# Optimization experiments

Hardware: AMD Instinct MI355X
Metric: run time of the kernel (lower is better)

The kernel has to match this reference:

```python
import jax, jax.numpy as jnp
import numpy as np


def setup_inputs() -> dict:
    key = jax.random.key(0)
    k1, k2, k3, k4 = jax.random.split(key, 4)
    N, M, D, C = 8192, 8192, 512, 128
    ref_feats = jax.random.normal(k1, (N, D), dtype=jnp.float32)
    src_feats = jax.random.normal(k2, (M, D), dtype=jnp.float32)
    # pairwise_distance(..., normalized=True) assumes unit-norm features
    ref_feats = ref_feats / jnp.linalg.norm(ref_feats, axis=-1, keepdims=True)
    src_feats = src_feats / jnp.linalg.norm(src_feats, axis=-1, keepdims=True)
    cas_score0 = jax.random.uniform(k3, (C, N), dtype=jnp.float32)
    cas_score1 = jax.random.uniform(k4, (C, M), dtype=jnp.float32)
    return {
        "ref_feats": ref_feats,
        "src_feats": src_feats,
        "cas_score0": cas_score0,
        "cas_score1": cas_score1,
        "num_correspondences": 256,
    }


def reference(ref_feats, src_feats, cas_score0, cas_score1, num_correspondences):
    # masks are None -> all superpoints kept, ref_indices/src_indices = arange
    N = ref_feats.shape[0]
    M = src_feats.shape[0]
    # pairwise_distance(normalized=True): d = 2 - 2 * <ref, src>
    inner = jnp.einsum('nd,md->nm', ref_feats, src_feats)
    matching_scores = jnp.exp(-(2.0 - 2.0 * inner))  # [N, M]
    # dual normalization (row-wise and col-wise)
    ref_ms = matching_scores / jnp.sum(matching_scores, axis=1, keepdims=True)
    src_ms = matching_scores / jnp.sum(matching_scores, axis=0, keepdims=True)
    matching_scores = ref_ms * src_ms
    # overlap matrix: [N, M]
    overlap = jnp.einsum('cn,cm->nm', cas_score0, cas_score1)
    matching_scores = matching_scores * overlap
    k = min(num_correspondences, N * M)
    corr_scores, corr_indices = jax.lax.top_k(matching_scores.reshape(-1), k)
    ref_corr_indices = corr_indices // M
    src_corr_indices = corr_indices % M
    return ref_corr_indices, src_corr_indices, corr_scores
```

## Files before the change

### kernel.cpp

```cpp
#include <hip/hip_runtime.h>
#include <algorithm>
#include <cstdint>

#define Nn 8192
#define Mm 8192
#define Dd 512
#define Cc 128

#define BT  128
#define TK  16

#define KERNEL_OCC __launch_bounds__(256, 2)

#define WS_SR    0ull
#define WS_SC    65536ull
#define WS_CTR   131072ull
#define WS_GHC   131136ull
#define WS_GHF   132160ull
#define WS_FINAL 133184ull
#define WS_CAND  165952ull
#define WS_INNER 25331776ull
#define RSTORE   7296
#define WS_NEED  (WS_INNER + (size_t)RSTORE * Mm * 4ull)
#define FCAP     4096u

__device__ __forceinline__ int jcol(int tx, int j) {
  return (j < 4) ? tx * 4 + j : 64 + tx * 4 + (j - 4);
}

__device__ __forceinline__ void inner_gemm(const float* __restrict__ A,
                                           const float* __restrict__ B,
                                           int n0, int m0, int tid,
                                           float (*SA)[BT], float (*SB)[BT],
                                           float acc2[8][8]) {
  const int tx = tid & 15, ty = tid >> 4;
  const int lrow = tid >> 1;
  const int lk8  = (tid & 1) * 8;
  const float* Ap = A + (size_t)(n0 + lrow) * Dd + lk8;
  const float* Bp = B + (size_t)(m0 + lrow) * Dd + lk8;

#pragma unroll
  for (int i = 0; i < 8; ++i)
#pragma unroll
    for (int j = 0; j < 8; ++j) acc2[i][j] = 0.0f;

  float4 pa0 = *(const float4*)(Ap);
  float4 pa1 = *(const float4*)(Ap + 4);
  float4 pb0 = *(const float4*)(Bp);
  float4 pb1 = *(const float4*)(Bp + 4);

  for (int k0 = 0; k0 < Dd; k0 += TK) {
    __syncthreads();
    {
      const float ar[8] = {pa0.x,pa0.y,pa0.z,pa0.w,pa1.x,pa1.y,pa1.z,pa1.w};
      const float br[8] = {pb0.x,pb0.y,pb0.z,pb0.w,pb1.x,pb1.y,pb1.z,pb1.w};
#pragma unroll
      for (int s = 0; s < 8; ++s) { SA[lk8 + s][lrow] = ar[s]; SB[lk8 + s][lrow] = br[s]; }
    }
    if (k0 + TK < Dd) {
      pa0 = *(const float4*)(Ap + k0 + TK);
      pa1 = *(const float4*)(Ap + k0 + TK + 4);
      pb0 = *(const float4*)(Bp + k0 + TK);
      pb1 = *(const float4*)(Bp + k0 + TK + 4);
    }
    __syncthreads();
#pragma unroll
    for (int h = 0; h < 2; ++h) {
      float t[4][8];
#pragma unroll
      for (int i = 0; i < 4; ++i)
#pragma unroll
        for (int j = 0; j < 8; ++j) t[i][j] = 0.0f;
#pragma unroll
      for (int kk = 0; kk < TK; ++kk) {
        const float4 av  = *(const float4*)&SA[kk][ty * 8 + h * 4];
        const float4 bv0 = *(const float4*)&SB[kk][tx * 4];
        const float4 bv1 = *(const float4*)&SB[kk][64 + tx * 4];
        const float a[4] = {av.x, av.y, av.z, av.w};
        const float b[8] = {bv0.x,bv0.y,bv0.z,bv0.w,bv1.x,bv1.y,bv1.z,bv1.w};
#pragma unroll
        for (int i = 0; i < 4; ++i)
#pragma unroll
          for (int j = 0; j < 8; ++j) t[i][j] = fmaf(a[i], b[j], t[i][j]);
      }
#pragma unroll
      for (int i = 0; i < 4; ++i)
#pragma unroll
        for (int j = 0; j < 8; ++j) acc2[h * 4 + i][j] += t[i][j];
    }
  }
}

template<bool STORE>
__global__ KERNEL_OCC void k_pass1(const float* __restrict__ A,
                                   const float* __restrict__ B,
                                   double* __restrict__ Sr,
                                   double* __restrict__ Sc,
                                   float* __restrict__ inner) {
  __shared__ float SA[TK][BT];
  __shared__ float SB[TK][BT];
  __shared__ double csum[BT];
  const int tid = threadIdx.x;
  const int tx = tid & 15, ty = tid >> 4;
  const int n0 = blockIdx.y * BT, m0 = blockIdx.x * BT;

  float acc2[8][8];
  inner_gemm(A, B, n0, m0, tid, SA, SB, acc2);

  if (STORE && n0 < RSTORE) {
#pragma unroll
    for (int i = 0; i < 8; ++i) {
      float* rowp = inner + (size_t)(n0 + ty * 8 + i) * Mm + m0;
      *(float4*)(rowp + tx * 4)      = make_float4(acc2[i][0], acc2[i][1], acc2[i][2], acc2[i][3]);
      *(float4*)(rowp + 64 + tx * 4) = make_float4(acc2[i][4], acc2[i][5], acc2[i][6], acc2[i][7]);
    }
  }

  if (tid < BT) csum[tid] = 0.0;
  __syncthreads();

  float cp[8];
#pragma unroll
  for (int j = 0; j < 8; ++j) cp[j] = 0.0f;

#pragma unroll
  for (int i = 0; i < 8; ++i) {
    float r = 0.0f;
#pragma unroll
    for (int j = 0; j < 8; ++j) {
      const float e = expf(2.0f * acc2[i][j] - 2.0f);
      r += e;
      cp[j] += e;
    }
    double v = (double)r;
    v += __shfl_xor(v, 1, 16);
    v += __shfl_xor(v, 2, 16);
    v += __shfl_xor(v, 4, 16);
    v += __shfl_xor(v, 8, 16);
    if (tx == 0) atomicAdd(&Sr[n0 + ty * 8 + i], v);
  }
#pragma unroll
  for (int j = 0; j < 8; ++j) {
    double v = (double)cp[j];
    v += __shfl_xor(v, 16, 64);
    v += __shfl_xor(v, 32, 64);
    if ((tid & 63) < 16) atomicAdd(&csum[jcol(tx, j)], v);
  }
  __syncthreads();
  if (tid < BT) atomicAdd(&Sc[m0 + tid], csum[tid]);
}

__global__ void k_recip(double* __restrict__ Sr, double* __restrict__ Sc) {
  const int i = blockIdx.x * 256 + threadIdx.x;
  if (i < Nn) Sr[i] = 1.0 / Sr[i];
  if (i < Mm) Sc[i] = 1.0 / Sc[i];
}

template<bool RELOAD>
__global__ KERNEL_OCC void k_pass2(
    const float* __restrict__ A, const float* __restrict__ B,
    const float* __restrict__ C0, const float* __restrict__ C1,
    const double* __restrict__ invSr, const double* __restrict__ invSc,
    const float* __restrict__ inner, int yoff,
    uint2* __restrict__ cand, unsigned int* __restrict__ ctr, unsigned int cap) {
  __shared__ float SA[TK][BT];
  __shared__ float SB[TK][BT];
  __shared__ unsigned int h1[256];
  __shared__ unsigned int wsum[4];
  __shared__ unsigned int sh_misc[4];
  __shared__ double dsr[BT];
  __shared__ double dsc[BT];
  const int tid = threadIdx.x;
  const int tx = tid & 15, ty = tid >> 4;
  const int n0 = (blockIdx.y + yoff) * BT, m0 = blockIdx.x * BT;

  if (tid < BT) dsr[tid] = invSr[n0 + tid];
  else          dsc[tid - BT] = invSc[m0 + tid - BT];

  float acc2[8][8];
  if (!RELOAD) {
    inner_gemm(A, B, n0, m0, tid, SA, SB, acc2);
  }

  const int frow = tid >> 4;
  const int fn   = (tid & 15) * 8;

#pragma unroll
  for (int h = 0; h < 2; ++h) {
    float ov[8][4];
#pragma unroll
    for (int i = 0; i < 8; ++i)
#pragma unroll
      for (int j = 0; j < 4; ++j) ov[i][j] = 0.0f;
    for (int c0i = 0; c0i < Cc; c0i += TK) {
      __syncthreads();
      *(float4*)&SA[frow][fn]     = *(const float4*)(C0 + (size_t)(c0i + frow) * Nn + n0 + fn);
      *(float4*)&SA[frow][fn + 4] = *(const float4*)(C0 + (size_t)(c0i + frow) * Nn + n0 + fn + 4);
      *(float4*)&SB[frow][fn]     = *(const float4*)(C1 + (size_t)(c0i + frow) * Mm + m0 + fn);
      *(float4*)&SB[frow][fn + 4] = *(const float4*)(C1 + (size_t)(c0i + frow) * Mm + m0 + fn + 4);
      __syncthreads();
#pragma unroll
      for (int g = 0; g < 2; ++g) {
        float th[4][4];
#pragma unroll
        for (int i = 0; i < 4; ++i)
#pragma unroll
          for (int j = 0; j < 4; ++j) th[i][j] = 0.0f;
#pragma unroll
        for (int kk = 0; kk < TK; ++kk) {
          const float4 av = *(const float4*)&SA[kk][ty * 8 + g * 4];
          const float4 bv = *(const float4*)&SB[kk][h * 64 + tx * 4];
          const float a[4] = {av.x, av.y, av.z, av.w};
          const float b[4] = {bv.x, bv.y, bv.z, bv.w};
#pragma unroll
          for (int i = 0; i < 4; ++i)
#pragma unroll
            for (int j = 0; j < 4; ++j) th[i][j] = fmaf(a[i], b[j], th[i][j]);
        }
#pragma unroll
        for (int i = 0; i < 4; ++i)
#pragma unroll
          for (int j = 0; j < 4; ++j) ov[g * 4 + i][j] += th[i][j];
      }
    }

    float acch[8][4];
    if (RELOAD) {
#pragma unroll
      for (int i = 0; i < 8; ++i)
        *(float4*)&acch[i][0] =
            *(const float4*)(inner + (size_t)(n0 + ty * 8 + i) * Mm + m0 + h * 64 + tx * 4);
    } else {
#pragma unroll
      for (int i = 0; i < 8; ++i)
#pragma unroll
        for (int j = 0; j < 4; ++j) acch[i][j] = acc2[i][h * 4 + j];
    }

    unsigned int sb[8][4];
#pragma unroll
    for (int i = 0; i < 8; ++i)
#pragma unroll
      for (int j = 0; j < 4; ++j) {
        const double e = exp(2.0 * (double)acch[i][j] - 2.0);
        const double s = e * e * dsr[ty * 8 + i] * dsc[h * 64 + tx * 4 + j] * (double)ov[i][j];
        sb[i][j] = __float_as_uint((float)s);
      }

    __syncthreads();
    h1[tid] = 0;
    __syncthreads();
#pragma unroll
    for (int i = 0; i < 8; ++i)
#pragma unroll
      for (int j = 0; j < 4; ++j) atomicAdd(&h1[sb[i][j] >> 24], 1u);
    __syncthreads();
    if (tid == 0) {
      unsigned cum = 0, cb2 = 0, abv = 0;
      for (int b = 255; b >= 0; --b) {
        const unsigned nc = cum + h1[b];
        if (nc >= 256u) { cb2 = (unsigned)b; abv = cum; break; }
        cum = nc;
      }
      sh_misc[0] = cb2; sh_misc[1] = abv;
    }
    __syncthreads();
    const unsigned cb = sh_misc[0], above = sh_misc[1];
    __syncthreads();
    h1[tid] = 0;
    __syncthreads();
#pragma unroll
    for (int i = 0; i < 8; ++i)
#pragma unroll
      for (int j = 0; j < 4; ++j)
        if ((sb[i][j] >> 24) == cb) atomicAdd(&h1[(sb[i][j] >> 16) & 0xFFu], 1u);
    __syncthreads();
    if (tid == 0) {
      unsigned cum = above, tb = cb << 8;
      for (int b = 255; b >= 0; --b) {
        cum += h1[b];
        if (cum >= 256u) { tb = (cb << 8) | (unsigned)b; break; }
      }
      const unsigned old = atomicMax(&ctr[2], tb);
      sh_misc[2] = tb > old ? tb : old;
    }
    __syncthreads();
    const unsigned tb16 = sh_misc[2];

    unsigned cnt = 0;
#pragma unroll
    for (int i = 0; i < 8; ++i)
#pragma unroll
      for (int j = 0; j < 4; ++j) cnt += ((sb[i][j] >> 16) >= tb16) ? 1u : 0u;
    const int lane = tid & 63, wv = tid >> 6;
    unsigned incl = cnt;
#pragma unroll
    for (int d = 1; d < 64; d <<= 1) {
      const unsigned nv = __shfl_up(incl, d, 64);
      if (lane >= d) incl += nv;
    }
    if (lane == 63) wsum[wv] = incl;
    __syncthreads();
    if (tid == 0) {
      unsigned run = 0;
#pragma unroll
      for (int w = 0; w < 4; ++w) { const unsigned c = wsum[w]; wsum[w] = run; run += c; }
      sh_misc[3] = atomicAdd(&ctr[0], run);
    }
    __syncthreads();
    unsigned pos = sh_misc[3] + wsum[wv] + incl - cnt;
#pragma unroll
    for (int i = 0; i < 8; ++i)
#pragma unroll
      for (int j = 0; j < 4; ++j) {
        if ((sb[i][j] >> 16) >= tb16) {
          if (pos < cap) {
            const unsigned idxv = ((unsigned)(n0 + ty * 8 + i) << 13)
                                | (unsigned)(m0 + h * 64 + tx * 4 + j);
            cand[pos] = make_uint2(sb[i][j], idxv);
          }
          ++pos;
        }
      }
    __syncthreads();
  }
}

__global__ __launch_bounds__(256) void k_histc(const uint2* __restrict__ cand,
                                               const unsigned int* __restrict__ ctr,
                                               unsigned int cap,
                                               unsigned int* __restrict__ ghc) {
  __shared__ unsigned int lh[256];
  const int tid = threadIdx.x;
  lh[tid] = 0;
  __syncthreads();
  const unsigned n = min(ctr[0], cap);
  const unsigned stride = gridDim.x * blockDim.x;
  for (unsigned i = blockIdx.x * blockDim.x + tid; i < n; i += stride)
    atomicAdd(&lh[cand[i].x >> 24], 1u);
  __syncthreads();
  if (lh[tid]) atomicAdd(&ghc[tid], lh[tid]);
}

__global__ __launch_bounds__(256) void k_threshc(const unsigned int* __restrict__ ghc,
                                                 unsigned int* __restrict__ ctr) {
  __shared__ unsigned int g[256];
  const int tid = threadIdx.x;
  g[tid] = ghc[tid];
  __syncthreads();
  if (tid == 0) {
    unsigned cum = 0;
    for (int b = 255; b >= 0; --b) {
      cum += g[b];
      if (cum >= 256u) { ctr[4] = (unsigned)b; ctr[5] = cum - g[b]; break; }
    }
  }
}

__global__ __launch_bounds__(256) void k_histf(const uint2* __restrict__ cand,
                                               const unsigned int* __restrict__ ctr,
                                               unsigned int cap,
                                               unsigned int* __restrict__ ghf) {
  __shared__ unsigned int lh[256];
  const int tid = threadIdx.x;
  lh[tid] = 0;
  __syncthreads();
  const unsigned n = min(ctr[0], cap);
  const unsigned cb = ctr[4];
  const unsigned stride = gridDim.x * blockDim.x;
  for (unsigned i = blockIdx.x * blockDim.x + tid; i < n; i += stride) {
    const unsigned k = cand[i].x;
    if ((k >> 24) == cb) atomicAdd(&lh[(k >> 16) & 0xFFu], 1u);
  }
  __syncthreads();
  if (lh[tid]) atomicAdd(&ghf[tid], lh[tid]);
}

__global__ __launch_bounds__(256) void k_threshf(const unsigned int* __restrict__ ghf,
                                                 unsigned int* __restrict__ ctr) {
  __shared__ unsigned int g[256];
  const int tid = threadIdx.x;
  g[tid] = ghf[tid];
  __syncthreads();
  if (tid == 0) {
    const unsigned cb = ctr[4];
    unsigned cum = ctr[5], tb = cb << 8;
    for (int b = 255; b >= 0; --b) {
      cum += g[b];
      if (cum >= 256u) { tb = (cb << 8) | (unsigned)b; break; }
    }
    ctr[3] = tb;
  }
}

__global__ void k_collect(const uint2* __restrict__ cand,
                          unsigned int* __restrict__ ctr,
                          unsigned int cap, uint2* __restrict__ fin) {
  const unsigned n = min(ctr[0], cap);
  const unsigned tb = ctr[3];
  const unsigned stride = gridDim.x * blockDim.x;
  for (unsigned i = blockIdx.x * blockDim.x + threadIdx.x; i < n; i += stride) {
    const uint2 c = cand[i];
    if ((c.x >> 16) >= tb) {
      const unsigned p = atomicAdd(&ctr[1], 1u);
      if (p < FCAP) fin[p] = c;
    }
  }
}

__global__ __launch_bounds__(256) void k_sort(const uint2* __restrict__ fin,
                                              const unsigned int* __restrict__ ctr,
                                              float* __restrict__ out) {
  __shared__ unsigned long long kk[FCAP];
  const int tid = threadIdx.x;
  const unsigned n = min(ctr[1], FCAP);
  unsigned np2 = 256;
  while (np2 < n) np2 <<= 1;
  for (unsigned i = tid; i < np2; i += 256) {
    if (i < n) {
      const uint2 c = fin[i];
      kk[i] = ((unsigned long long)c.x << 32) | (unsigned long long)(c.y ^ 0xFFFFFFFFu);
    } else {
      kk[i] = 0ull;
    }
  }
  __syncthreads();
  for (unsigned k2 = 2; k2 <= np2; k2 <<= 1) {
    for (unsigned j = k2 >> 1; j > 0; j >>= 1) {
      for (unsigned i = tid; i < np2; i += 256) {
        const unsigned l = i ^ j;
        if (l > i) {
          const unsigned long long ka = kk[i], kb = kk[l];
          const bool aBefore = ka > kb;
          const bool dsc = (i & k2) == 0;
          const bool sw = dsc ? !aBefore : aBefore;
          if (sw) { kk[i] = kb; kk[l] = ka; }
        }
      }
      __syncthreads();
    }
  }
  {
    const unsigned long long kv = kk[tid];
    const unsigned key = (unsigned)(kv >> 32);
    const unsigned ix  = ((unsigned)kv) ^ 0xFFFFFFFFu;
    out[tid]        = (float)(ix >> 13);
    out[256 + tid]  = (float)(ix & 8191u);
    out[512 + tid]  = __uint_as_float(key);
  }
}

extern "C" void kernel_launch(void* const* d_in, const int* in_sizes, int n_in,
                              void* d_out, int out_size, void* d_ws, size_t ws_size,
                              hipStream_t stream) {
  (void)in_sizes; (void)n_in; (void)out_size;
  const float* ref = (const float*)d_in[0];
  const float* src = (const float*)d_in[1];
  const float* c0  = (const float*)d_in[2];
  const float* c1  = (const float*)d_in[3];
  char* ws = (char*)d_ws;
  double* Sr = (double*)(ws + WS_SR);
  double* Sc = (double*)(ws + WS_SC);
  unsigned int* ctr = (unsigned int*)(ws + WS_CTR);
  unsigned int* ghc = (unsigned int*)(ws + WS_GHC);
  unsigned int* ghf = (unsigned int*)(ws + WS_GHF);
  uint2* fin   = (uint2*)(ws + WS_FINAL);
  uint2* cand  = (uint2*)(ws + WS_CAND);
  float* inner = (float*)(ws + WS_INNER);

  const bool store = ws_size >= (size_t)WS_NEED;
  unsigned int cap;
  if (store) {
    cap = (unsigned int)((WS_INNER - WS_CAND) / 8);
  } else {
    cap = (ws_size > WS_CAND + 8)
        ? (unsigned int)std::min<size_t>((ws_size - WS_CAND) / 8, (size_t)(16u << 20))
        : 0u;
  }

  hipMemsetAsync(d_ws, 0, (size_t)WS_FINAL, stream);

  dim3 g1(Mm / BT, Nn / BT);
  if (store) {
    k_pass1<true><<<g1, 256, 0, stream>>>(ref, src, Sr, Sc, inner);
    k_recip<<<32, 256, 0, stream>>>(Sr, Sc);
    dim3 gre(Mm / BT, RSTORE / BT);
    dim3 grc(Mm / BT, (Nn - RSTORE) / BT);
    k_pass2<true><<<gre, 256, 0, stream>>>(ref, src, c0, c1, Sr, Sc, inner, 0, cand, ctr, cap);
    k_pass2<false><<<grc, 256, 0, stream>>>(ref, src, c0, c1, Sr, Sc, nullptr, RSTORE / BT, cand, ctr, cap);
  } else {
    k_pass1<false><<<g1, 256, 0, stream>>>(ref, src, Sr, Sc, nullptr);
    k_recip<<<32, 256, 0, stream>>>(Sr, Sc);
    k_pass2<false><<<g1, 256, 0, stream>>>(ref, src, c0, c1, Sr, Sc, nullptr, 0, cand, ctr, cap);
  }
  k_histc<<<256, 256, 0, stream>>>(cand, ctr, cap, ghc);
  k_threshc<<<1, 256, 0, stream>>>(ghc, ctr);
  k_histf<<<256, 256, 0, stream>>>(cand, ctr, cap, ghf);
  k_threshf<<<1, 256, 0, stream>>>(ghf, ctr);
  k_collect<<<256, 256, 0, stream>>>(cand, ctr, cap, fin);
  k_sort<<<1, 256, 0, stream>>>(fin, ctr, (float*)d_out);
}
```

Before: 1.958 ms.

## Double-buffer GEMM shared tiles and parallelize per-block top-k histogram scans

Shared-memory staging for the inner-product GEMM becomes double-buffered, which removes one barrier per k-step. In the reload path the overlap GEMM is computed once over the full 128x128 tile with register prefetch and double buffering, where before it was recomputed per half. The serial single-thread histogram scans in the candidate threshold selection become a 64-lane suffix scan with a ballot, and a second histogram buffer removes extra barriers. This costs more shared memory, which could reduce occupancy, and more registers for the 8x8 overlap accumulator.

```diff
diff --git a/kernel.cpp b/kernel.cpp
--- a/kernel.cpp
+++ b/kernel.cpp
@@ -31,7 +31,7 @@
 __device__ __forceinline__ void inner_gemm(const float* __restrict__ A,
                                            const float* __restrict__ B,
                                            int n0, int m0, int tid,
-                                           float (*SA)[BT], float (*SB)[BT],
+                                           float (*SA)[TK][BT], float (*SB)[TK][BT],
                                            float acc2[8][8]) {
   const int tx = tid & 15, ty = tid >> 4;
   const int lrow = tid >> 1;
@@ -49,13 +49,13 @@
   float4 pb0 = *(const float4*)(Bp);
   float4 pb1 = *(const float4*)(Bp + 4);
 
+  int p = 0;
   for (int k0 = 0; k0 < Dd; k0 += TK) {
-    __syncthreads();
     {
       const float ar[8] = {pa0.x,pa0.y,pa0.z,pa0.w,pa1.x,pa1.y,pa1.z,pa1.w};
       const float br[8] = {pb0.x,pb0.y,pb0.z,pb0.w,pb1.x,pb1.y,pb1.z,pb1.w};
 #pragma unroll
-      for (int s = 0; s < 8; ++s) { SA[lk8 + s][lrow] = ar[s]; SB[lk8 + s][lrow] = br[s]; }
+      for (int s = 0; s < 8; ++s) { SA[p][lk8 + s][lrow] = ar[s]; SB[p][lk8 + s][lrow] = br[s]; }
     }
     if (k0 + TK < Dd) {
       pa0 = *(const float4*)(Ap + k0 + TK);
@@ -73,9 +73,9 @@
         for (int j = 0; j < 8; ++j) t[i][j] = 0.0f;
 #pragma unroll
       for (int kk = 0; kk < TK; ++kk) {
-        const float4 av  = *(const float4*)&SA[kk][ty * 8 + h * 4];
-        const float4 bv0 = *(const float4*)&SB[kk][tx * 4];
-        const float4 bv1 = *(const float4*)&SB[kk][64 + tx * 4];
+        const float4 av  = *(const float4*)&SA[p][kk][ty * 8 + h * 4];
+        const float4 bv0 = *(const float4*)&SB[p][kk][tx * 4];
+        const float4 bv1 = *(const float4*)&SB[p][kk][64 + tx * 4];
         const float a[4] = {av.x, av.y, av.z, av.w};
         const float b[8] = {bv0.x,bv0.y,bv0.z,bv0.w,bv1.x,bv1.y,bv1.z,bv1.w};
 #pragma unroll
@@ -88,6 +88,7 @@
 #pragma unroll
         for (int j = 0; j < 8; ++j) acc2[h * 4 + i][j] += t[i][j];
     }
+    p ^= 1;
   }
 }
 
@@ -97,8 +98,8 @@
                                    double* __restrict__ Sr,
                                    double* __restrict__ Sc,
                                    float* __restrict__ inner) {
-  __shared__ float SA[TK][BT];
-  __shared__ float SB[TK][BT];
+  __shared__ float SA[2][TK][BT];
+  __shared__ float SB[2][TK][BT];
   __shared__ double csum[BT];
   const int tid = threadIdx.x;
   const int tx = tid & 15, ty = tid >> 4;
@@ -154,6 +155,115 @@
   const int i = blockIdx.x * 256 + threadIdx.x;
   if (i < Nn) Sr[i] = 1.0 / Sr[i];
   if (i < Mm) Sc[i] = 1.0 / Sc[i];
+}
+
+__device__ __forceinline__ void select_push(const unsigned (*sb)[4],
+                                            int n0, int m0, int hh, int tid,
+                                            unsigned int* h1, unsigned int* h2,
+                                            unsigned int* wsum, unsigned int* sh_misc,
+                                            uint2* __restrict__ cand,
+                                            unsigned int* __restrict__ ctr,
+                                            unsigned int cap) {
+  const int tx = tid & 15, ty = tid >> 4;
+
+  h1[tid] = 0; h2[tid] = 0;
+  __syncthreads();
+#pragma unroll
+  for (int i = 0; i < 8; ++i)
+#pragma unroll
+    for (int j = 0; j < 4; ++j) atomicAdd(&h1[sb[i][j] >> 24], 1u);
+  __syncthreads();
+  if (tid < 64) {
+    const int b0 = tid * 4;
+    const unsigned s4 = h1[b0] + h1[b0 + 1] + h1[b0 + 2] + h1[b0 + 3];
+    unsigned suf = s4;
+#pragma unroll
+    for (int d = 1; d < 64; d <<= 1) {
+      const unsigned v = __shfl_down(suf, d, 64);
+      if (tid + d < 64) suf += v;
+    }
+    const unsigned long long mk = __ballot(suf >= 256u);
+    const int L = 63 - __builtin_clzll(mk);
+    if (tid == L) {
+      unsigned cum = suf - s4;
+      unsigned cb = (unsigned)(4 * L), abv = cum;
+      for (int b = 4 * L + 3; b >= 4 * L; --b) {
+        const unsigned nc = cum + h1[b];
+        if (nc >= 256u) { cb = (unsigned)b; abv = cum; break; }
+        cum = nc;
+      }
+      sh_misc[0] = cb; sh_misc[1] = abv;
+    }
+  }
+  __syncthreads();
+  const unsigned cb = sh_misc[0], above = sh_misc[1];
+#pragma unroll
+  for (int i = 0; i < 8; ++i)
+#pragma unroll
+    for (int j = 0; j < 4; ++j)
+      if ((sb[i][j] >> 24) == cb) atomicAdd(&h2[(sb[i][j] >> 16) & 0xFFu], 1u);
+  __syncthreads();
+  if (tid < 64) {
+    const int b0 = tid * 4;
+    const unsigned s4 = h2[b0] + h2[b0 + 1] + h2[b0 + 2] + h2[b0 + 3];
+    unsigned suf = s4;
+#pragma unroll
+    for (int d = 1; d < 64; d <<= 1) {
+      const unsigned v = __shfl_down(suf, d, 64);
+      if (tid + d < 64) suf += v;
+    }
+    const unsigned long long mk = __ballot(above + suf >= 256u);
+    const int L = 63 - __builtin_clzll(mk);
+    if (tid == L) {
+      unsigned cum = above + suf - s4;
+      unsigned tb = cb << 8;
+      for (int b = 4 * L + 3; b >= 4 * L; --b) {
+        cum += h2[b];
+        if (cum >= 256u) { tb = (cb << 8) | (unsigned)b; break; }
+      }
+      const unsigned old = atomicMax(&ctr[2], tb);
+      sh_misc[2] = tb > old ? tb : old;
+    }
+  }
+  __syncthreads();
+  const unsigned tb16 = sh_misc[2];
+
+  unsigned cnt = 0;
+#pragma unroll
+  for (int i = 0; i < 8; ++i)
+#pragma unroll
+    for (int j = 0; j < 4; ++j) cnt += ((sb[i][j] >> 16) >= tb16) ? 1u : 0u;
+  const int lane = tid & 63, wv = tid >> 6;
+  unsigned incl = cnt;
+#pragma unroll
+  for (int d = 1; d < 64; d <<= 1) {
+    const unsigned nv = __shfl_up(incl, d, 64);
+    if (lane >= d) incl += nv;
+  }
+  if (lane == 63) wsum[wv] = incl;
+  __syncthreads();
+  if (tid == 0) {
+    unsigned run = 0;
+#pragma unroll
+    for (int w = 0; w < 4; ++w) { const unsigned c = wsum[w]; wsum[w] = run; run += c; }
+    sh_misc[3] = atomicAdd(&ctr[0], run);
+  }
+  __syncthreads();
+  unsigned pos = sh_misc[3] + wsum[wv] + incl - cnt;
+#pragma unroll
+  for (int i = 0; i < 8; ++i)
+#pragma unroll
+    for (int j = 0; j < 4; ++j) {
+      if ((sb[i][j] >> 16) >= tb16) {
+        if (pos < cap) {
+          const unsigned idxv = ((unsigned)(n0 + ty * 8 + i) << 13)
+                              | (unsigned)(m0 + hh * 64 + tx * 4 + j);
+          cand[pos] = make_uint2(sb[i][j], idxv);
+        }
+        ++pos;
+      }
+    }
+  __syncthreads();
 }
 
 template<bool RELOAD>
@@ -163,9 +273,10 @@
     const double* __restrict__ invSr, const double* __restrict__ invSc,
     const float* __restrict__ inner, int yoff,
     uint2* __restrict__ cand, unsigned int* __restrict__ ctr, unsigned int cap) {
-  __shared__ float SA[TK][BT];
-  __shared__ float SB[TK][BT];
+  __shared__ float SA[2][TK][BT];
+  __shared__ float SB[2][TK][BT];
   __shared__ unsigned int h1[256];
+  __shared__ unsigned int h2[256];
   __shared__ unsigned int wsum[4];
   __shared__ unsigned int sh_misc[4];
   __shared__ double dsr[BT];
@@ -177,152 +288,137 @@
   if (tid < BT) dsr[tid] = invSr[n0 + tid];
   else          dsc[tid - BT] = invSc[m0 + tid - BT];
 
-  float acc2[8][8];
-  if (!RELOAD) {
-    inner_gemm(A, B, n0, m0, tid, SA, SB, acc2);
-  }
-
   const int frow = tid >> 4;
   const int fn   = (tid & 15) * 8;
 
-#pragma unroll
-  for (int h = 0; h < 2; ++h) {
-    float ov[8][4];
+  if (RELOAD) {
+    float ov[8][8];
 #pragma unroll
     for (int i = 0; i < 8; ++i)
 #pragma unroll
-      for (int j = 0; j < 4; ++j) ov[i][j] = 0.0f;
+      for (int j = 0; j < 8; ++j) ov[i][j] = 0.0f;
+
+    const float* c0p = C0 + (size_t)frow * Nn + n0 + fn;
+    const float* c1p = C1 + (size_t)frow * Mm + m0 + fn;
+    float4 ca0 = *(const float4*)(c0p);
+    float4 ca1 = *(const float4*)(c0p + 4);
+    float4 cb0 = *(const float4*)(c1p);
+    float4 cb1 = *(const float4*)(c1p + 4);
+    int p = 0;
     for (int c0i = 0; c0i < Cc; c0i += TK) {
+      *(float4*)&SA[p][frow][fn]     = ca0;
+      *(float4*)&SA[p][frow][fn + 4] = ca1;
+      *(float4*)&SB[p][frow][fn]     = cb0;
+      *(float4*)&SB[p][frow][fn + 4] = cb1;
+      if (c0i + TK < Cc) {
+        const size_t off = (size_t)(c0i + TK);
+        ca0 = *(const float4*)(c0p + off * Nn);
+        ca1 = *(const float4*)(c0p + off * Nn + 4);
+        cb0 = *(const float4*)(c1p + off * Mm);
+        cb1 = *(const float4*)(c1p + off * Mm + 4);
+      }
       __syncthreads();
-      *(float4*)&SA[frow][fn]     = *(const float4*)(C0 + (size_t)(c0i + frow) * Nn + n0 + fn);
-      *(float4*)&SA[frow][fn + 4] = *(const float4*)(C0 + (size_t)(c0i + frow) * Nn + n0 + fn + 4);
-      *(float4*)&SB[frow][fn]     = *(const float4*)(C1 + (size_t)(c0i + frow) * Mm + m0 + fn);
-      *(float4*)&SB[frow][fn + 4] = *(const float4*)(C1 + (size_t)(c0i + frow) * Mm + m0 + fn + 4);
-      __syncthreads();
-#pragma unroll
-      for (int g = 0; g < 2; ++g) {
-        float th[4][4];
-#pragma unroll
-        for (int i = 0; i < 4; ++i)
-#pragma unroll
-          for (int j = 0; j < 4; ++j) th[i][j] = 0.0f;
-#pragma unroll
-        for (int kk = 0; kk < TK; ++kk) {
-          const float4 av = *(const float4*)&SA[kk][ty * 8 + g * 4];
-          const float4 bv = *(const float4*)&SB[kk][h * 64 + tx * 4];
-          const float a[4] = {av.x, av.y, av.z, av.w};
-          const float b[4] = {bv.x, bv.y, bv.z, bv.w};
+#pragma unroll
+      for (int g = 0; g < 2; ++g)
+#pragma unroll
+        for (int u = 0; u < 2; ++u) {
+          float th[4][4];
 #pragma unroll
           for (int i = 0; i < 4; ++i)
 #pragma unroll
-            for (int j = 0; j < 4; ++j) th[i][j] = fmaf(a[i], b[j], th[i][j]);
+            for (int j = 0; j < 4; ++j) th[i][j] = 0.0f;
+#pragma unroll
+          for (int kk = 0; kk < TK; ++kk) {
+            const float4 av = *(const float4*)&SA[p][kk][ty * 8 + g * 4];
+            const float4 bv = *(const float4*)&SB[p][kk][u * 64 + tx * 4];
+            const float a[4] = {av.x, av.y, av.z, av.w};
+            const float b[4] = {bv.x, bv.y, bv.z, bv.w};
+#pragma unroll
+            for (int i = 0; i < 4; ++i)
+#pragma unroll
+              for (int j = 0; j < 4; ++j) th[i][j] = fmaf(a[i], b[j], th[i][j]);
+          }
+#pragma unroll
+          for (int i = 0; i < 4; ++i)
+#pragma unroll
+            for (int j = 0; j < 4; ++j) ov[g * 4 + i][u * 4 + j] += th[i][j];
         }
-#pragma unroll
-        for (int i = 0; i < 4; ++i)
-#pragma unroll
-          for (int j = 0; j < 4; ++j) ov[g * 4 + i][j] += th[i][j];
-      }
-    }
-
-    float acch[8][4];
-    if (RELOAD) {
+      p ^= 1;
+    }
+
+#pragma unroll 1
+    for (int hh = 0; hh < 2; ++hh) {
+      unsigned sb[8][4];
+#pragma unroll
+      for (int i = 0; i < 8; ++i) {
+        const float4 ar = *(const float4*)(inner + (size_t)(n0 + ty * 8 + i) * Mm
+                                           + m0 + hh * 64 + tx * 4);
+        const float a4[4] = {ar.x, ar.y, ar.z, ar.w};
+#pragma unroll
+        for (int j = 0; j < 4; ++j) {
+          const double e = exp(2.0 * (double)a4[j] - 2.0);
+          const double s = e * e * dsr[ty * 8 + i] * dsc[hh * 64 + tx * 4 + j]
+                         * (double)ov[i][hh * 4 + j];
+          sb[i][j] = __float_as_uint((float)s);
+        }
+      }
+      select_push(sb, n0, m0, hh, tid, h1, h2, wsum, sh_misc, cand, ctr, cap);
+    }
+  } else {
+    float acc2[8][8];
+    inner_gemm(A, B, n0, m0, tid, SA, SB, acc2);
+
+#pragma unroll 1
+    for (int hh = 0; hh < 2; ++hh) {
+      float ov[8][4];
 #pragma unroll
       for (int i = 0; i < 8; ++i)
-        *(float4*)&acch[i][0] =
-            *(const float4*)(inner + (size_t)(n0 + ty * 8 + i) * Mm + m0 + h * 64 + tx * 4);
-    } else {
+#pragma unroll
+        for (int j = 0; j < 4; ++j) ov[i][j] = 0.0f;
+      for (int c0i = 0; c0i < Cc; c0i += TK) {
+        __syncthreads();
+        *(float4*)&SA[0][frow][fn]     = *(const float4*)(C0 + (size_t)(c0i + frow) * Nn + n0 + fn);
+        *(float4*)&SA[0][frow][fn + 4] = *(const float4*)(C0 + (size_t)(c0i + frow) * Nn + n0 + fn + 4);
+        *(float4*)&SB[0][frow][fn]     = *(const float4*)(C1 + (size_t)(c0i + frow) * Mm + m0 + fn);
+        *(float4*)&SB[0][frow][fn + 4] = *(const float4*)(C1 + (size_t)(c0i + frow) * Mm + m0 + fn + 4);
+        __syncthreads();
+#pragma unroll
+        for (int g = 0; g < 2; ++g) {
+          float th[4][4];
+#pragma unroll
+          for (int i = 0; i < 4; ++i)
+#pragma unroll
+            for (int j = 0; j < 4; ++j) th[i][j] = 0.0f;
+#pragma unroll
+          for (int kk = 0; kk < TK; ++kk) {
+            const float4 av = *(const float4*)&SA[0][kk][ty * 8 + g * 4];
+            const float4 bv = *(const float4*)&SB[0][kk][hh * 64 + tx * 4];
+            const float a[4] = {av.x, av.y, av.z, av.w};
+            const float b[4] = {bv.x, bv.y, bv.z, bv.w};
+#pragma unroll
+            for (int i = 0; i < 4; ++i)
+#pragma unroll
+              for (int j = 0; j < 4; ++j) th[i][j] = fmaf(a[i], b[j], th[i][j]);
+          }
+#pragma unroll
+          for (int i = 0; i < 4; ++i)
+#pragma unroll
+            for (int j = 0; j < 4; ++j) ov[g * 4 + i][j] += th[i][j];
+        }
+      }
+
+      unsigned sb[8][4];
 #pragma unroll
       for (int i = 0; i < 8; ++i)
 #pragma unroll
-        for (int j = 0; j < 4; ++j) acch[i][j] = acc2[i][h * 4 + j];
-    }
-
-    unsigned int sb[8][4];
-#pragma unroll
-    for (int i = 0; i < 8; ++i)
-#pragma unroll
-      for (int j = 0; j < 4; ++j) {
-        const double e = exp(2.0 * (double)acch[i][j] - 2.0);
-        const double s = e * e * dsr[ty * 8 + i] * dsc[h * 64 + tx * 4 + j] * (double)ov[i][j];
-        sb[i][j] = __float_as_uint((float)s);
-      }
-
-    __syncthreads();
-    h1[tid] = 0;
-    __syncthreads();
-#pragma unroll
-    for (int i = 0; i < 8; ++i)
-#pragma unroll
-      for (int j = 0; j < 4; ++j) atomicAdd(&h1[sb[i][j] >> 24], 1u);
-    __syncthreads();
-    if (tid == 0) {
-      unsigned cum = 0, cb2 = 0, abv = 0;
-      for (int b = 255; b >= 0; --b) {
-        const unsigned nc = cum + h1[b];
-        if (nc >= 256u) { cb2 = (unsigned)b; abv = cum; break; }
-        cum = nc;
-      }
-      sh_misc[0] = cb2; sh_misc[1] = abv;
-    }
-    __syncthreads();
-    const unsigned cb = sh_misc[0], above = sh_misc[1];
-    __syncthreads();
-    h1[tid] = 0;
-    __syncthreads();
-#pragma unroll
-    for (int i = 0; i < 8; ++i)
-#pragma unroll
-      for (int j = 0; j < 4; ++j)
-        if ((sb[i][j] >> 24) == cb) atomicAdd(&h1[(sb[i][j] >> 16) & 0xFFu], 1u);
-    __syncthreads();
-    if (tid == 0) {
-      unsigned cum = above, tb = cb << 8;
-      for (int b = 255; b >= 0; --b) {
-        cum += h1[b];
-        if (cum >= 256u) { tb = (cb << 8) | (unsigned)b; break; }
-      }
-      const unsigned old = atomicMax(&ctr[2], tb);
-      sh_misc[2] = tb > old ? tb : old;
-    }
-    __syncthreads();
-    const unsigned tb16 = sh_misc[2];
-
-    unsigned cnt = 0;
-#pragma unroll
-    for (int i = 0; i < 8; ++i)
-#pragma unroll
-      for (int j = 0; j < 4; ++j) cnt += ((sb[i][j] >> 16) >= tb16) ? 1u : 0u;
-    const int lane = tid & 63, wv = tid >> 6;
-    unsigned incl = cnt;
-#pragma unroll
-    for (int d = 1; d < 64; d <<= 1) {
-      const unsigned nv = __shfl_up(incl, d, 64);
-      if (lane >= d) incl += nv;
-    }
-    if (lane == 63) wsum[wv] = incl;
-    __syncthreads();
-    if (tid == 0) {
-      unsigned run = 0;
-#pragma unroll
-      for (int w = 0; w < 4; ++w) { const unsigned c = wsum[w]; wsum[w] = run; run += c; }
-      sh_misc[3] = atomicAdd(&ctr[0], run);
-    }
-    __syncthreads();
-    unsigned pos = sh_misc[3] + wsum[wv] + incl - cnt;
-#pragma unroll
-    for (int i = 0; i < 8; ++i)
-#pragma unroll
-      for (int j = 0; j < 4; ++j) {
-        if ((sb[i][j] >> 16) >= tb16) {
-          if (pos < cap) {
-            const unsigned idxv = ((unsigned)(n0 + ty * 8 + i) << 13)
-                                | (unsigned)(m0 + h * 64 + tx * 4 + j);
-            cand[pos] = make_uint2(sb[i][j], idxv);
-          }
-          ++pos;
+        for (int j = 0; j < 4; ++j) {
+          const double e = exp(2.0 * (double)acc2[i][hh * 4 + j] - 2.0);
+          const double s = e * e * dsr[ty * 8 + i] * dsc[hh * 64 + tx * 4 + j]
+                         * (double)ov[i][j];
+          sb[i][j] = __float_as_uint((float)s);
         }
-      }
-    __syncthreads();
+      select_push(sb, n0, m0, hh, tid, h1, h2, wsum, sh_misc, cand, ctr, cap);
+    }
   }
 }
 
```

New measurement: 4.247 ms. 117% more time.
